# Performance work log

Hardware: AMD Instinct MI355X
Metric: run time of the kernel (lower is better)

## Reference

```python
import jax, jax.numpy as jnp
import numpy as np

N_NODES = 20000
N_EDGES = 640000
IN_FEATS, H_FEATS, N_CLASSES = 300, 512, 256


def setup_inputs() -> dict:
    key = jax.random.key(0)
    ks = jax.random.split(key, 8)
    x = jax.random.normal(ks[0], (N_NODES, IN_FEATS), dtype=jnp.float32)
    # Glorot-ish scaling for weights
    W_self1 = jax.random.normal(ks[1], (IN_FEATS, H_FEATS), dtype=jnp.float32) / np.sqrt(IN_FEATS)
    W_neigh1 = jax.random.normal(ks[2], (IN_FEATS, H_FEATS), dtype=jnp.float32) / np.sqrt(IN_FEATS)
    b1 = jnp.zeros((H_FEATS,), dtype=jnp.float32)
    W_self2 = jax.random.normal(ks[3], (H_FEATS, N_CLASSES), dtype=jnp.float32) / np.sqrt(H_FEATS)
    W_neigh2 = jax.random.normal(ks[4], (H_FEATS, N_CLASSES), dtype=jnp.float32) / np.sqrt(H_FEATS)
    b2 = jnp.zeros((N_CLASSES,), dtype=jnp.float32)
    src = jax.random.randint(ks[5], (N_EDGES,), 0, N_NODES, dtype=jnp.int32)
    dst = jax.random.randint(ks[6], (N_EDGES,), 0, N_NODES, dtype=jnp.int32)
    return {"x": x, "W_self1": W_self1, "W_neigh1": W_neigh1, "b1": b1,
            "W_self2": W_self2, "W_neigh2": W_neigh2, "b2": b2,
            "src": src, "dst": dst}


def _mean_aggregate(h, src, dst):
    # mean of in-neighbor (src) features per destination node
    summed = jax.ops.segment_sum(h[src], dst, num_segments=N_NODES)  # [N, d]
    deg = jax.ops.segment_sum(jnp.ones_like(dst, dtype=h.dtype), dst, num_segments=N_NODES)
    return summed / jnp.maximum(deg, 1.0)[:, None]


def _sage_conv(h, src, dst, W_self, W_neigh, b):
    # DGL SAGEConv('mean'): fc_self(h) + fc_neigh(mean_neighbors(h)) + bias
    h_neigh = _mean_aggregate(h, src, dst)
    return h @ W_self + h_neigh @ W_neigh + b


def reference(x, W_self1, W_neigh1, b1, W_self2, W_neigh2, b2, src, dst):
    h = _sage_conv(x, src, dst, W_self1, W_neigh1, b1)
    h = jax.nn.relu(h)
    h = _sage_conv(h, src, dst, W_self2, W_neigh2, b2)
    return h
```

## Files before the change

### kernel.cpp

```cpp
#include <hip/hip_runtime.h>


typedef _Float16 f16;
typedef _Float16 f16x4 __attribute__((ext_vector_type(4)));
typedef _Float16 f16x8 __attribute__((ext_vector_type(8)));
typedef float f32x4 __attribute__((ext_vector_type(4)));

constexpr int NN = 20000;
constexpr int NE = 640000;
constexpr int F0 = 300;
constexpr int F1 = 512;
constexpr int F2 = 256;
constexpr int KP1 = 640;
constexpr int XOFF = 320;

__device__ __forceinline__ int xcd_swz(int b, int nb) {
    int xcd = b & 7, loc = b >> 3;
    int q = nb >> 3, r = nb & 7;
    return (xcd < r ? xcd * (q + 1) : r * (q + 1) + (xcd - r) * q) + loc;
}

__global__ void conv_x_kernel(const float* __restrict__ x, f16* __restrict__ A1b) {
    long idx = (long)blockIdx.x * 256 + threadIdx.x;
    if (idx >= (long)NN * 80) return;
    int m = (int)(idx / 80), c = (int)(idx % 80);
    if (c < 75) {
        float4 v = *(const float4*)(x + (long)m * F0 + 4 * c);
        f16x4 h = {(f16)v.x, (f16)v.y, (f16)v.z, (f16)v.w};
        *(f16x4*)(A1b + (long)m * KP1 + 4 * c) = h;
    } else {
        f16x4 z = {};
        *(f16x4*)(A1b + (long)m * KP1 + 300 + (c - 75) * 4) = z;
    }
}

__global__ void prep_w1_kernel(const float* __restrict__ Ws1, const float* __restrict__ Wn1,
                               f16* __restrict__ Wt1) {
    int idx = blockIdx.x * 256 + threadIdx.x;
    if (idx >= F1 * KP1) return;
    int n = idx / KP1, k = idx % KP1;
    float v = 0.f;
    if (k < 300) v = Ws1[k * F1 + n];
    else if (k >= XOFF && k < XOFF + 300) v = Wn1[(k - XOFF) * F1 + n];
    Wt1[idx] = (f16)v;
}

__global__ void prep_w2cat_kernel(const float* __restrict__ Ws2, const float* __restrict__ Wn2,
                                  f16* __restrict__ Wt) {
    int idx = blockIdx.x * 256 + threadIdx.x;
    if (idx >= 2 * F2 * F1) return;
    int n = idx / F1, k = idx % F1;
    float v = (n < F2) ? Wn2[k * F2 + n] : Ws2[k * F2 + (n - F2)];
    Wt[idx] = (f16)v;
}

__global__ void count_kernel(const int* __restrict__ dst, int* __restrict__ cnt) {
    int e = blockIdx.x * 256 + threadIdx.x;
    if (e < NE) atomicAdd(&cnt[dst[e]], 1);
}

__global__ __launch_bounds__(1024) void scan_kernel(const int* __restrict__ cnt,
                                                    int* __restrict__ row_ptr,
                                                    int* __restrict__ cursor) {
    constexpr int CH = (NN + 1023) / 1024;
    __shared__ int part[1024];
    const int t = threadIdx.x;
    int base = t * CH;
    int s = 0;
    #pragma unroll
    for (int i = 0; i < CH; ++i) {
        int idx = base + i;
        if (idx < NN) s += cnt[idx];
    }
    part[t] = s;
    __syncthreads();
    #pragma unroll
    for (int off = 1; off < 1024; off <<= 1) {
        int v = (t >= off) ? part[t - off] : 0;
        __syncthreads();
        part[t] += v;
        __syncthreads();
    }
    int run = (t == 0) ? 0 : part[t - 1];
    #pragma unroll
    for (int i = 0; i < CH; ++i) {
        int idx = base + i;
        if (idx < NN) {
            row_ptr[idx] = run;
            cursor[idx] = run;
            run += cnt[idx];
        }
    }
    if (t == 1023) row_ptr[NN] = part[1023];
}

__global__ void fill_kernel(const int* __restrict__ src, const int* __restrict__ dst,
                            int* __restrict__ cursor, int* __restrict__ csr_src) {
    int e = blockIdx.x * 256 + threadIdx.x;
    if (e >= NE) return;
    int pos = atomicAdd(&cursor[dst[e]], 1);
    csr_src[pos] = src[e];
}


__global__ __launch_bounds__(256) void gather1_kernel(const int* __restrict__ row_ptr,
                                                      const int* __restrict__ csr,
                                                      f16* __restrict__ A1b) {
    int wid = xcd_swz(blockIdx.x, 5 * 625);
    int seg = wid / 625;
    int g = (wid % 625) * 256 + threadIdx.x;
    int m = g >> 3;
    int off = seg * 64 + (g & 7) * 8;
    int beg = row_ptr[m], end = row_ptr[m + 1];
    float a[8] = {};
    for (int e = beg; e < end; ++e) {
        int s = csr[e];
        f16x8 v = *(const f16x8*)(A1b + (long)s * KP1 + off);
        #pragma unroll
        for (int j = 0; j < 8; ++j) a[j] += (float)v[j];
    }
    float inv = 1.0f / fmaxf((float)(end - beg), 1.0f);
    f16x8 w;
    #pragma unroll
    for (int j = 0; j < 8; ++j) w[j] = (f16)(a[j] * inv);
    *(f16x8*)(A1b + (long)m * KP1 + XOFF + off) = w;
}

__global__ __launch_bounds__(256) void gather2_kernel(const int* __restrict__ row_ptr,
                                                      const int* __restrict__ csr,
                                                      const f16* __restrict__ t2,
                                                      const float* __restrict__ self,
                                                      float* __restrict__ out) {
    int wid = xcd_swz(blockIdx.x, 4 * 625);
    int seg = wid / 625;
    int g = (wid % 625) * 256 + threadIdx.x;
    int m = g >> 3;
    int off = seg * 64 + (g & 7) * 8;
    int beg = row_ptr[m], end = row_ptr[m + 1];
    float a[8] = {};
    for (int e = beg; e < end; ++e) {
        int s = csr[e];
        f16x8 v = *(const f16x8*)(t2 + (long)s * F2 + off);
        #pragma unroll
        for (int j = 0; j < 8; ++j) a[j] += (float)v[j];
    }
    float inv = 1.0f / fmaxf((float)(end - beg), 1.0f);
    const float* sp = self + (long)m * F2 + off;
    f32x4 s0 = *(const f32x4*)(sp);
    f32x4 s1 = *(const f32x4*)(sp + 4);
    f32x4 w0 = {a[0]*inv + s0[0], a[1]*inv + s0[1], a[2]*inv + s0[2], a[3]*inv + s0[3]};
    f32x4 w1 = {a[4]*inv + s1[0], a[5]*inv + s1[1], a[6]*inv + s1[2], a[7]*inv + s1[3]};
    float* op = out + (long)m * F2 + off;
    *(f32x4*)(op) = w0;
    *(f32x4*)(op + 4) = w1;
}

template<int MODE>
__global__ __launch_bounds__(256) void hgemm_kernel(
    const f16* __restrict__ A, const f16* __restrict__ Bt,
    const float* __restrict__ bias, float* __restrict__ out_f32,
    f16* __restrict__ out_f16, int M, int N, int K)
{
    __shared__ f16 As[64][72];
    __shared__ f16 Bs[128][72];

    const int t = threadIdx.x;
    const int lane = t & 63, wave = t >> 6;
    const int wr = wave >> 1, wc = wave & 1;
    const int m0 = blockIdx.x * 64, n0 = blockIdx.y * 128;
    const int ar = t >> 2, ac = (t & 3) * 16;
    const int br = t >> 1, bc = (t & 1) * 32;

    f32x4 acc[2][4] = {};

    for (int k0 = 0; k0 < K; k0 += 64) {
        {
            const f16* ga = A + (long)(m0 + ar) * K + k0 + ac;
            bool mok = (m0 + ar) < M;
            f16x8 v0 = mok ? *(const f16x8*)(ga + 0) : (f16x8){};
            f16x8 v1 = mok ? *(const f16x8*)(ga + 8) : (f16x8){};
            *(f16x8*)&As[ar][ac + 0] = v0;
            *(f16x8*)&As[ar][ac + 8] = v1;
        }
        {
            const f16* gb = Bt + (long)(n0 + br) * K + k0 + bc;
            f16x8 v0 = *(const f16x8*)(gb + 0);
            f16x8 v1 = *(const f16x8*)(gb + 8);
            f16x8 v2 = *(const f16x8*)(gb + 16);
            f16x8 v3 = *(const f16x8*)(gb + 24);
            *(f16x8*)&Bs[br][bc + 0]  = v0;
            *(f16x8*)&Bs[br][bc + 8]  = v1;
            *(f16x8*)&Bs[br][bc + 16] = v2;
            *(f16x8*)&Bs[br][bc + 24] = v3;
        }
        __syncthreads();
        #pragma unroll
        for (int kk = 0; kk < 2; ++kk) {
            f16x8 af[2], bf[4];
            #pragma unroll
            for (int i = 0; i < 2; ++i)
                af[i] = *(const f16x8*)&As[wr * 32 + i * 16 + (lane & 15)][kk * 32 + (lane >> 4) * 8];
            #pragma unroll
            for (int j = 0; j < 4; ++j)
                bf[j] = *(const f16x8*)&Bs[wc * 64 + j * 16 + (lane & 15)][kk * 32 + (lane >> 4) * 8];
            #pragma unroll
            for (int i = 0; i < 2; ++i)
                #pragma unroll
                for (int j = 0; j < 4; ++j)
                    acc[i][j] = __builtin_amdgcn_mfma_f32_16x16x32_f16(af[i], bf[j], acc[i][j], 0, 0, 0);
        }
        __syncthreads();
    }

    const int cr = (lane >> 4) * 4, cc = lane & 15;
    #pragma unroll
    for (int i = 0; i < 2; ++i) {
        #pragma unroll
        for (int j = 0; j < 4; ++j) {
            int n = n0 + wc * 64 + j * 16 + cc;
            float b;
            if (MODE == 1) b = bias[n];
            else           b = (n >= F2) ? bias[n - F2] : 0.f;
            #pragma unroll
            for (int q = 0; q < 4; ++q) {
                int m = m0 + wr * 32 + i * 16 + cr + q;
                if (m >= M) continue;
                float v = acc[i][j][q];
                if (MODE == 1) {
                    out_f16[(long)m * N + n] = (f16)fmaxf(v + b, 0.f);
                } else {
                    if (n < F2) out_f16[(long)m * F2 + n] = (f16)v;
                    else        out_f32[(long)m * F2 + (n - F2)] = v + b;
                }
            }
        }
    }
}

extern "C" void kernel_launch(void* const* d_in, const int* in_sizes, int n_in,
                              void* d_out, int out_size, void* d_ws, size_t ws_size,
                              hipStream_t stream) {
    const float* x   = (const float*)d_in[0];
    const float* Ws1 = (const float*)d_in[1];
    const float* Wn1 = (const float*)d_in[2];
    const float* b1  = (const float*)d_in[3];
    const float* Ws2 = (const float*)d_in[4];
    const float* Wn2 = (const float*)d_in[5];
    const float* b2  = (const float*)d_in[6];
    const int* src   = (const int*)d_in[7];
    const int* dst   = (const int*)d_in[8];
    float* out = (float*)d_out;

    char* ws = (char*)d_ws;
    int* row_ptr = (int*)(ws);
    int* csr_src = (int*)(ws + 80064);
    int* cursor  = (int*)(ws + 2640064);
    f16* A1b     = (f16*)(ws + 2720064);
    f16* h1      = (f16*)(ws + 28320064);
    f16* t2      = (f16*)(ws + 48800064);
    float* selfp = (float*)(ws + 59040064);
    f16* Wt1     = (f16*)(ws + 79520064);
    f16* Wt2cat  = (f16*)(ws + 80175424);

    conv_x_kernel<<<(int)(((long)NN * 80) / 256), 256, 0, stream>>>(x, A1b);
    prep_w1_kernel<<<(F1 * KP1) / 256, 256, 0, stream>>>(Ws1, Wn1, Wt1);
    prep_w2cat_kernel<<<(2 * F2 * F1) / 256, 256, 0, stream>>>(Ws2, Wn2, Wt2cat);

    hipMemsetAsync(cursor, 0, NN * sizeof(int), stream);
    count_kernel<<<(NE + 255) / 256, 256, 0, stream>>>(dst, cursor);
    scan_kernel<<<1, 1024, 0, stream>>>(cursor, row_ptr, cursor);
    fill_kernel<<<(NE + 255) / 256, 256, 0, stream>>>(src, dst, cursor, csr_src);

    gather1_kernel<<<5 * 625, 256, 0, stream>>>(row_ptr, csr_src, A1b);
    dim3 g1((NN + 63) / 64, F1 / 128);
    hgemm_kernel<1><<<g1, 256, 0, stream>>>(A1b, Wt1, b1, nullptr, h1, NN, F1, KP1);

    dim3 g2((NN + 63) / 64, (2 * F2) / 128);
    hgemm_kernel<2><<<g2, 256, 0, stream>>>(h1, Wt2cat, b2, selfp, t2, NN, 2 * F2, F1);
    gather2_kernel<<<4 * 625, 256, 0, stream>>>(row_ptr, csr_src, t2, selfp, out);
}
```

Baseline: 417.1 us.

## Partition gathers by XCD feature window and swizzle GEMM tiles across XCDs

Result: slower. 433.4 us (+3.9%).

```diff
diff --git a/kernel.cpp b/kernel.cpp
--- a/kernel.cpp
+++ b/kernel.cpp
@@ -106,23 +106,24 @@
 __global__ __launch_bounds__(256) void gather1_kernel(const int* __restrict__ row_ptr,
                                                       const int* __restrict__ csr,
                                                       f16* __restrict__ A1b) {
-    int wid = xcd_swz(blockIdx.x, 5 * 625);
-    int seg = wid / 625;
-    int g = (wid % 625) * 256 + threadIdx.x;
+    int win = blockIdx.x & 7;
+    int g = (blockIdx.x >> 3) * 256 + threadIdx.x;
+    int j = g & 7;
+    if (j >= 5) return;
     int m = g >> 3;
-    int off = seg * 64 + (g & 7) * 8;
+    int off = win * 40 + j * 8;
     int beg = row_ptr[m], end = row_ptr[m + 1];
     float a[8] = {};
     for (int e = beg; e < end; ++e) {
         int s = csr[e];
         f16x8 v = *(const f16x8*)(A1b + (long)s * KP1 + off);
         #pragma unroll
-        for (int j = 0; j < 8; ++j) a[j] += (float)v[j];
+        for (int k = 0; k < 8; ++k) a[k] += (float)v[k];
     }
     float inv = 1.0f / fmaxf((float)(end - beg), 1.0f);
     f16x8 w;
     #pragma unroll
-    for (int j = 0; j < 8; ++j) w[j] = (f16)(a[j] * inv);
+    for (int k = 0; k < 8; ++k) w[k] = (f16)(a[k] * inv);
     *(f16x8*)(A1b + (long)m * KP1 + XOFF + off) = w;
 }
 
@@ -131,18 +132,18 @@
                                                       const f16* __restrict__ t2,
                                                       const float* __restrict__ self,
                                                       float* __restrict__ out) {
-    int wid = xcd_swz(blockIdx.x, 4 * 625);
-    int seg = wid / 625;
-    int g = (wid % 625) * 256 + threadIdx.x;
-    int m = g >> 3;
-    int off = seg * 64 + (g & 7) * 8;
+    int win = blockIdx.x & 7;
+    int g = (blockIdx.x >> 3) * 256 + threadIdx.x;
+    int m = g >> 2;
+    if (m >= NN) return;
+    int off = win * 32 + (g & 3) * 8;
     int beg = row_ptr[m], end = row_ptr[m + 1];
     float a[8] = {};
     for (int e = beg; e < end; ++e) {
         int s = csr[e];
         f16x8 v = *(const f16x8*)(t2 + (long)s * F2 + off);
         #pragma unroll
-        for (int j = 0; j < 8; ++j) a[j] += (float)v[j];
+        for (int k = 0; k < 8; ++k) a[k] += (float)v[k];
     }
     float inv = 1.0f / fmaxf((float)(end - beg), 1.0f);
     const float* sp = self + (long)m * F2 + off;
@@ -159,15 +160,17 @@
 __global__ __launch_bounds__(256) void hgemm_kernel(
     const f16* __restrict__ A, const f16* __restrict__ Bt,
     const float* __restrict__ bias, float* __restrict__ out_f32,
-    f16* __restrict__ out_f16, int M, int N, int K)
+    f16* __restrict__ out_f16, int M, int N, int K, int nb)
 {
     __shared__ f16 As[64][72];
     __shared__ f16 Bs[128][72];
 
+    const int wid = xcd_swz(blockIdx.x, nb);
+    const int m0 = (wid >> 2) * 64, n0 = (wid & 3) * 128;
+
     const int t = threadIdx.x;
     const int lane = t & 63, wave = t >> 6;
     const int wr = wave >> 1, wc = wave & 1;
-    const int m0 = blockIdx.x * 64, n0 = blockIdx.y * 128;
     const int ar = t >> 2, ac = (t & 3) * 16;
     const int br = t >> 1, bc = (t & 1) * 32;
 
@@ -271,11 +274,9 @@
     scan_kernel<<<1, 1024, 0, stream>>>(cursor, row_ptr, cursor);
     fill_kernel<<<(NE + 255) / 256, 256, 0, stream>>>(src, dst, cursor, csr_src);
 
-    gather1_kernel<<<5 * 625, 256, 0, stream>>>(row_ptr, csr_src, A1b);
-    dim3 g1((NN + 63) / 64, F1 / 128);
-    hgemm_kernel<1><<<g1, 256, 0, stream>>>(A1b, Wt1, b1, nullptr, h1, NN, F1, KP1);
-
-    dim3 g2((NN + 63) / 64, (2 * F2) / 128);
-    hgemm_kernel<2><<<g2, 256, 0, stream>>>(h1, Wt2cat, b2, selfp, t2, NN, 2 * F2, F1);
-    gather2_kernel<<<4 * 625, 256, 0, stream>>>(row_ptr, csr_src, t2, selfp, out);
-}
+    gather1_kernel<<<8 * 625, 256, 0, stream>>>(row_ptr, csr_src, A1b);
+    hgemm_kernel<1><<<313 * 4, 256, 0, stream>>>(A1b, Wt1, b1, nullptr, h1, NN, F1, KP1, 313 * 4);
+
+    hgemm_kernel<2><<<313 * 4, 256, 0, stream>>>(h1, Wt2cat, b2, selfp, t2, NN, 2 * F2, F1, 313 * 4);
+    gather2_kernel<<<8 * 313, 256, 0, stream>>>(row_ptr, csr_src, t2, selfp, out);
+}
```
